# Kernel optimization log

Measured on AMD Instinct MI355X. Metric: run time of the kernel, lower is better.

The kernel has to match this reference:

```python
import jax, jax.numpy as jnp
import numpy as np

N = 20000   # nodes
E = 160000  # edges
D = 128     # out_dim == in_dim
H = 8       # heads
DK = D // H # 16


def setup_inputs() -> dict:
    key = jax.random.key(0)
    ks = jax.random.split(key, 16)
    f = lambda i, shape, s=1.0: jax.random.normal(ks[i], shape, dtype=jnp.float32) * s
    z = lambda shape: jnp.zeros(shape, dtype=jnp.float32)
    return {
        "x_txt": f(0, (N, D)), "x_img": f(1, (N, D)), "x_s": f(2, (N, D)),
        "Wk": f(3, (D, D), 0.05), "bk": z((D,)),
        "Wq": f(4, (D, D), 0.05), "bq": z((D,)),
        "Wv": f(5, (D, D), 0.05), "bv": z((D,)),
        "Wa": f(6, (D, D), 0.05), "ba": z((D,)),
        "rel_att": f(7, (H, DK, DK), 0.25),
        "rel_msg": f(8, (H, DK, DK), 0.25),
        "rel_pri": jnp.ones((H,), jnp.float32),
        "wm_txt": f(9, (H, DK, DK), 0.25),
        "wm_img": f(10, (H, DK, DK), 0.25),
        "wm_s": f(11, (H, DK, DK), 0.25),
        "skip": jnp.ones((1,), jnp.float32),
        "src": jax.random.randint(ks[12], (E,), 0, N),
        "dst": jax.random.randint(ks[13], (E,), 0, N),
    }


def reference(x_txt, x_img, x_s, Wk, bk, Wq, bq, Wv, bv, Wa, ba,
              rel_att, rel_msg, rel_pri, wm_txt, wm_img, wm_s, skip, src, dst):
    n_heads, dk = rel_att.shape[0], rel_att.shape[1]
    n_nodes = x_txt.shape[0]
    sqrt_dk = jnp.sqrt(jnp.asarray(dk, jnp.float32))

    def proj(x, W, b):
        return (x @ W + b).reshape(n_nodes, n_heads, dk)

    xs = (x_txt, x_img, x_s)
    k = [proj(x, Wk, bk)[src] for x in xs]  # [E,H,dk] gathered at src
    q = [proj(x, Wq, bq)[dst] for x in xs]  # [E,H,dk] gathered at dst
    v = [proj(x, Wv, bv)[src] for x in xs]

    # cross-modal lambda: per-edge modality alignment softmax (over the 3 modalities)
    wm = (wm_txt, wm_img, wm_s)
    lam_scores = jnp.stack(
        [jnp.einsum('ehd,hdf,ehf->eh', k[m], wm[m], q[m]) for m in range(3)], axis=0)
    lam = jax.nn.softmax(lam_scores, axis=0)  # [3,E,H]

    # edge attention logits (scaled *10 as in reduce_func) and relation-msg values
    att = [jnp.einsum('ehd,hdf,ehf->eh', k[m], rel_att, q[m]) * rel_pri / sqrt_dk * 10.0
           for m in range(3)]
    vmsg = [jnp.einsum('ehd,hdf->ehf', v[m], rel_msg) for m in range(3)]

    align = -(jnp.abs(att[0] - att[1]) + jnp.abs(att[0] - att[2])
              + jnp.abs(att[1] - att[2])) / 3.0

    def seg_softmax(x):  # softmax over edges sharing the same dst node
        m = jax.ops.segment_max(x, dst, num_segments=n_nodes)
        m = jnp.where(jnp.isfinite(m), m, 0.0)
        e = jnp.exp(x - m[dst])
        s = jax.ops.segment_sum(e, dst, num_segments=n_nodes)
        s = jnp.where(s == 0.0, 1.0, s)
        return e / s[dst]

    beta2 = seg_softmax(align)
    sm = [seg_softmax(a) for a in att]
    beta1 = sm[0] * lam[0] + sm[1] * lam[1] + sm[2] * lam[2]
    beta = seg_softmax(beta1 * beta2)  # [E,H]

    alpha = jax.nn.sigmoid(skip)  # [1]
    outs = []
    for m in range(3):
        h = jax.ops.segment_sum(beta[..., None] * vmsg[m], dst,
                                num_segments=n_nodes).reshape(n_nodes, -1)
        outs.append((h @ Wa + ba) * alpha + xs[m] * (1.0 - alpha))
    return tuple(outs)
```

## Files before the change

### kernel.cpp

```cpp
#include <hip/hip_runtime.h>

#define D 128
#define NH 8

typedef __bf16 bf16x8 __attribute__((ext_vector_type(8)));
typedef unsigned short ushortx8 __attribute__((ext_vector_type(8)));
typedef float floatx4 __attribute__((ext_vector_type(4)));

__device__ __forceinline__ float bf2f(unsigned short u) {
  union { unsigned int i; float f; } x; x.i = ((unsigned int)u) << 16; return x.f;
}
__device__ __forceinline__ unsigned short f2bf(float f) {
  union { float f; unsigned int i; } x; x.f = f;
  unsigned int i = x.i;
  return (unsigned short)((i + 0x7FFFu + ((i >> 16) & 1u)) >> 16);
}
__device__ __forceinline__ void acc2(unsigned int ku, unsigned int qu, float& s) {
  union { unsigned int i; float f; } a, b;
  a.i = ku << 16;          b.i = qu << 16;          s += a.f * b.f;
  a.i = ku & 0xffff0000u;  b.i = qu & 0xffff0000u;  s += a.f * b.f;
}

__device__ __forceinline__ void fold_item(
    int gid,
    const float* __restrict__ Wk, const float* __restrict__ bk,
    const float* __restrict__ Wq, const float* __restrict__ bq,
    const float* __restrict__ Wv, const float* __restrict__ bv,
    const float* __restrict__ rel_att, const float* __restrict__ rel_msg,
    const float* __restrict__ rel_pri,
    const float* __restrict__ wm0, const float* __restrict__ wm1,
    const float* __restrict__ wm2,
    unsigned short* __restrict__ Wt_all, float* __restrict__ bias_all)
{
  int p = gid >> 14;
  int idx = gid & 16383;
  int c = idx >> 7, k = idx & 127;
  int h = c >> 4, r = c & 15;
  float wsum = 0.f, bsum = 0.f;
  if (p == 0) {
    wsum = Wk[k * 128 + c];
    bsum = bk[c];
  } else if (p <= 4) {
    const float* M = (p == 1) ? rel_att : ((p == 2) ? wm0 : ((p == 3) ? wm1 : wm2));
#pragma unroll
    for (int f = 0; f < 16; f++) {
      float mv = M[h * 256 + r * 16 + f];
      wsum += Wq[k * 128 + h * 16 + f] * mv;
      bsum += bq[h * 16 + f] * mv;
    }
    if (p == 1) { float sc = rel_pri[h] * 2.5f; wsum *= sc; bsum *= sc; }
  } else {
#pragma unroll
    for (int d = 0; d < 16; d++) {
      float mv = rel_msg[h * 256 + d * 16 + r];
      wsum += Wv[k * 128 + h * 16 + d] * mv;
      bsum += bv[h * 16 + d] * mv;
    }
  }
  Wt_all[(size_t)p * 16384 + c * 128 + k] = f2bf(wsum);
  if (k == 0) bias_all[p * 128 + c] = bsum;
}

__device__ __forceinline__ void proj_tile(
    int t, const float* __restrict__ x0, const float* __restrict__ x1,
    const float* __restrict__ x2,
    const unsigned short* __restrict__ Wt_all, const float* __restrict__ bias_all,
    unsigned short* __restrict__ P, int N, unsigned short* Wt, int tid)
{
  int m = t % 3, rt = t / 3;
  const float* X = (m == 0) ? x0 : ((m == 1) ? x1 : x2);
  int wave = tid >> 6, lane = tid & 63;
  int quad = lane >> 4, l16 = lane & 15;
  int row0 = rt * 64 + wave * 16;
  int arow = row0 + l16; if (arow >= N) arow = N - 1;
  const float* ap = X + (size_t)arow * D;
  bf16x8 afr[4];
#pragma unroll
  for (int kk4 = 0; kk4 < 4; kk4++) {
    float4 f0 = *(const float4*)(ap + kk4 * 32 + quad * 8);
    float4 f1 = *(const float4*)(ap + kk4 * 32 + quad * 8 + 4);
    ushortx8 uu;
    uu[0]=f2bf(f0.x); uu[1]=f2bf(f0.y); uu[2]=f2bf(f0.z); uu[3]=f2bf(f0.w);
    uu[4]=f2bf(f1.x); uu[5]=f2bf(f1.y); uu[6]=f2bf(f1.z); uu[7]=f2bf(f1.w);
    afr[kk4] = __builtin_bit_cast(bf16x8, uu);
  }
  int r = row0 + l16;
  for (int pt = 0; pt < 4; pt++) {
    int wp = (pt == 0) ? 0 : ((pt == 1) ? 1 : ((pt == 2) ? (2 + m) : 5));
    const unsigned short* Wsrc = Wt_all + (size_t)wp * 16384;
    const float* B = bias_all + wp * 128;
    unsigned short* Pout = P + (size_t)(pt * 3 + m) * N * D;
    __syncthreads();
#pragma unroll
    for (int it = 0; it < 8; it++) {
      int idx = it * 256 + tid;
      int c = idx >> 4, kc = (idx & 15) << 3;
      *(uint4*)(&Wt[c * 136 + kc]) = *(const uint4*)(&Wsrc[c * 128 + kc]);
    }
    __syncthreads();
    floatx4 acc[8];
#pragma unroll
    for (int ct = 0; ct < 8; ct++) acc[ct] = (floatx4)0.f;
#pragma unroll
    for (int kk4 = 0; kk4 < 4; kk4++) {
#pragma unroll
      for (int ct2 = 0; ct2 < 8; ct2++) {
        uint4 bu = *(const uint4*)(&Wt[(ct2 * 16 + l16) * 136 + kk4 * 32 + quad * 8]);
        bf16x8 bf = __builtin_bit_cast(bf16x8, bu);
        acc[ct2] =
            __builtin_amdgcn_mfma_f32_16x16x32_bf16(bf, afr[kk4], acc[ct2], 0, 0, 0);
      }
    }
    if (r < N) {
      unsigned short* Prow = Pout + (size_t)r * D;
#pragma unroll
      for (int ct2 = 0; ct2 < 8; ct2++) {
        int colb = ct2 * 16 + quad * 4;
        float4 bi = *(const float4*)(&B[colb]);
        unsigned int lo = ((unsigned int)f2bf(acc[ct2][1] + bi.y) << 16) |
                          f2bf(acc[ct2][0] + bi.x);
        unsigned int hi = ((unsigned int)f2bf(acc[ct2][3] + bi.w) << 16) |
                          f2bf(acc[ct2][2] + bi.z);
        uint2 pk; pk.x = lo; pk.y = hi;
        *(uint2*)(&Prow[colb]) = pk;
      }
    }
  }
}

__device__ __forceinline__ void assign_chunk(
    int a, const int* __restrict__ counts, int* __restrict__ row_start,
    int* __restrict__ cursor, int* __restrict__ allocg, int N, int lane)
{
  int n = a * 64 + lane;
  int cnt = (n < N) ? counts[n] : 0;
  int x = cnt;
#pragma unroll
  for (int off = 1; off < 64; off <<= 1) {
    int y = __shfl_up(x, off, 64);
    if (lane >= off) x += y;
  }
  int wtot = __shfl(x, 63, 64);
  int wbase = 0;
  if (lane == 63) wbase = atomicAdd(allocg, wtot);
  wbase = __shfl(wbase, 63, 64);
  if (n < N) { int v = wbase + x - cnt; row_start[n] = v; cursor[n] = v; }
}

__device__ __forceinline__ void edge_vals(
    const unsigned short* __restrict__ P, size_t Nsz, int s, int h,
    const uint4 (&qa)[3][2], const uint4 (&qw)[3][2],
    float (&av)[3], float (&lv)[3])
{
#pragma unroll
  for (int m = 0; m < 3; m++) {
    const unsigned short* kp = P + ((size_t)m * Nsz + s) * 128 + h * 16;
    uint4 k0 = *(const uint4*)kp, k1 = *(const uint4*)(kp + 8);
    const unsigned int* ka = (const unsigned int*)&k0;
    const unsigned int* kb = (const unsigned int*)&k1;
    const unsigned int* a0 = (const unsigned int*)&qa[m][0];
    const unsigned int* a1 = (const unsigned int*)&qa[m][1];
    const unsigned int* w0 = (const unsigned int*)&qw[m][0];
    const unsigned int* w1 = (const unsigned int*)&qw[m][1];
    float da = 0.f, dw = 0.f;
#pragma unroll
    for (int j = 0; j < 4; j++) {
      acc2(ka[j], a0[j], da); acc2(kb[j], a1[j], da);
      acc2(ka[j], w0[j], dw); acc2(kb[j], w1[j], dw);
    }
    av[m] = da;
    lv[m] = dw;
  }
  float mx = fmaxf(lv[0], fmaxf(lv[1], lv[2]));
  float e0 = __expf(lv[0] - mx), e1 = __expf(lv[1] - mx), e2 = __expf(lv[2] - mx);
  float inv = 1.f / (e0 + e1 + e2);
  lv[0] = e0 * inv; lv[1] = e1 * inv; lv[2] = e2 * inv;
}

__device__ __forceinline__ void node_one(
    int n, const unsigned short* __restrict__ P,
    const int* __restrict__ row_start, const int* __restrict__ counts,
    const int* __restrict__ srcs, unsigned short* __restrict__ hagg,
    int N, int lane)
{
  int ro = row_start[n];
  int deg = counts[n];
  float acc00 = 0, acc01 = 0, acc10 = 0, acc11 = 0, acc20 = 0, acc21 = 0;
  if (deg > 0) {
    int h = lane & 7, slot = lane >> 3;
    size_t Nsz = (size_t)N;
    uint4 qa[3][2], qw[3][2];
#pragma unroll
    for (int m = 0; m < 3; m++) {
      const unsigned short* qap = P + ((size_t)(3 + m) * Nsz + n) * 128 + h * 16;
      const unsigned short* qwp = P + ((size_t)(6 + m) * Nsz + n) * 128 + h * 16;
      qa[m][0] = *(const uint4*)qap; qa[m][1] = *(const uint4*)(qap + 8);
      qw[m][0] = *(const uint4*)qwp; qw[m][1] = *(const uint4*)(qwp + 8);
    }
    int nch = (deg + 7) >> 3;
    float cX0[4] = {}, cX1[4] = {}, cX2[4] = {}, cEa[4] = {}, cT[4] = {};
    int cS[4] = {};
    float sA0 = 0, sA1 = 0, sA2 = 0, sAl = 0;
#pragma unroll
    for (int c = 0; c < 4; c++) {
      int idx = c * 8 + slot;
      if (c < nch && idx < deg) {
        int s = srcs[ro + idx]; cS[c] = s;
        float av[3], lv[3];
        edge_vals(P, Nsz, s, h, qa, qw, av, lv);
        float e0 = __expf(av[0]), e1 = __expf(av[1]), e2 = __expf(av[2]);
        float align = -(fabsf(av[0]-av[1]) + fabsf(av[0]-av[2]) + fabsf(av[1]-av[2])) * (1.f/3.f);
        float ea = __expf(align);
        cX0[c] = lv[0] * e0; cX1[c] = lv[1] * e1; cX2[c] = lv[2] * e2; cEa[c] = ea;
        sA0 += e0; sA1 += e1; sA2 += e2; sAl += ea;
      }
    }
    for (int c = 4; c < nch; c++) {
      int idx = c * 8 + slot;
      if (idx < deg) {
        int s = srcs[ro + idx];
        float av[3], lv[3];
        edge_vals(P, Nsz, s, h, qa, qw, av, lv);
        float align = -(fabsf(av[0]-av[1]) + fabsf(av[0]-av[2]) + fabsf(av[1]-av[2])) * (1.f/3.f);
        sA0 += __expf(av[0]); sA1 += __expf(av[1]); sA2 += __expf(av[2]);
        sAl += __expf(align);
      }
    }
#pragma unroll
    for (int off = 8; off < 64; off <<= 1) {
      sA0 += __shfl_xor(sA0, off, 64);
      sA1 += __shfl_xor(sA1, off, 64);
      sA2 += __shfl_xor(sA2, off, 64);
      sAl += __shfl_xor(sAl, off, 64);
    }
    float rA0 = 1.f / fmaxf(sA0, 1e-30f), rA1 = 1.f / fmaxf(sA1, 1e-30f);
    float rA2 = 1.f / fmaxf(sA2, 1e-30f), rAl = 1.f / fmaxf(sAl, 1e-30f);
    float sT = 0;
#pragma unroll
    for (int c = 0; c < 4; c++) {
      int idx = c * 8 + slot;
      if (c < nch && idx < deg) {
        float t = (cX0[c] * rA0 + cX1[c] * rA1 + cX2[c] * rA2) * (cEa[c] * rAl);
        cT[c] = t;
        sT += __expf(t);
      }
    }
    for (int c = 4; c < nch; c++) {
      int idx = c * 8 + slot;
      if (idx < deg) {
        int s = srcs[ro + idx];
        float av[3], lv[3];
        edge_vals(P, Nsz, s, h, qa, qw, av, lv);
        float align = -(fabsf(av[0]-av[1]) + fabsf(av[0]-av[2]) + fabsf(av[1]-av[2])) * (1.f/3.f);
        float t = (lv[0]*__expf(av[0])*rA0 + lv[1]*__expf(av[1])*rA1 + lv[2]*__expf(av[2])*rA2)
                  * (__expf(align) * rAl);
        sT += __expf(t);
      }
    }
#pragma unroll
    for (int off = 8; off < 64; off <<= 1) sT += __shfl_xor(sT, off, 64);
    float rT = 1.f / fmaxf(sT, 1e-30f);
    const unsigned int* Pu = (const unsigned int*)P;
    int hl = lane >> 3;
#pragma unroll
    for (int c = 0; c < 4; c++) {
      if (c < nch) {
        int idx = c * 8 + slot;
        float beta = (idx < deg) ? __expf(cT[c]) * rT : 0.f;
        int sv = cS[c];
        float bj[8]; int sj[8];
#pragma unroll
        for (int jj = 0; jj < 8; jj++) {
          bj[jj] = __shfl(beta, jj * 8 + hl, 64);
          sj[jj] = __shfl(sv, jj * 8, 64);
        }
#pragma unroll
        for (int jj = 0; jj < 8; jj++) {
          size_t base9 = ((size_t)9 * Nsz + sj[jj]) * 64 + lane;
          unsigned int u0 = Pu[base9];
          unsigned int u1 = Pu[base9 + Nsz * 64];
          unsigned int u2 = Pu[base9 + 2 * Nsz * 64];
          float b = bj[jj];
          acc00 += b * bf2f((unsigned short)u0); acc01 += b * bf2f((unsigned short)(u0 >> 16));
          acc10 += b * bf2f((unsigned short)u1); acc11 += b * bf2f((unsigned short)(u1 >> 16));
          acc20 += b * bf2f((unsigned short)u2); acc21 += b * bf2f((unsigned short)(u2 >> 16));
        }
      }
    }
    for (int c = 4; c < nch; c++) {
      int idx = c * 8 + slot;
      float beta = 0.f; int sv = 0;
      if (idx < deg) {
        sv = srcs[ro + idx];
        float av[3], lv[3];
        edge_vals(P, Nsz, sv, h, qa, qw, av, lv);
        float align = -(fabsf(av[0]-av[1]) + fabsf(av[0]-av[2]) + fabsf(av[1]-av[2])) * (1.f/3.f);
        float t = (lv[0]*__expf(av[0])*rA0 + lv[1]*__expf(av[1])*rA1 + lv[2]*__expf(av[2])*rA2)
                  * (__expf(align) * rAl);
        beta = __expf(t) * rT;
      }
      int jmax = min(8, deg - c * 8);
      for (int jj = 0; jj < jmax; jj++) {
        float b = __shfl(beta, jj * 8 + hl, 64);
        int s = __shfl(sv, jj * 8, 64);
        size_t base9 = ((size_t)9 * Nsz + s) * 64 + lane;
        unsigned int u0 = Pu[base9];
        unsigned int u1 = Pu[base9 + Nsz * 64];
        unsigned int u2 = Pu[base9 + 2 * Nsz * 64];
        acc00 += b * bf2f((unsigned short)u0); acc01 += b * bf2f((unsigned short)(u0 >> 16));
        acc10 += b * bf2f((unsigned short)u1); acc11 += b * bf2f((unsigned short)(u1 >> 16));
        acc20 += b * bf2f((unsigned short)u2); acc21 += b * bf2f((unsigned short)(u2 >> 16));
      }
    }
  }
  unsigned int* ho = (unsigned int*)hagg;
  ho[((size_t)0 * N + n) * 64 + lane] = ((unsigned int)f2bf(acc01) << 16) | f2bf(acc00);
  ho[((size_t)1 * N + n) * 64 + lane] = ((unsigned int)f2bf(acc11) << 16) | f2bf(acc10);
  ho[((size_t)2 * N + n) * 64 + lane] = ((unsigned int)f2bf(acc21) << 16) | f2bf(acc20);
}

__device__ __forceinline__ void out_tile(
    int t, const unsigned short* __restrict__ Hagg,
    const float* __restrict__ ba,
    const float* __restrict__ x0, const float* __restrict__ x1,
    const float* __restrict__ x2, float alpha,
    float* __restrict__ out, int N, const unsigned short* Wt, int tid)
{
  int m = t % 3, rt = t / 3;
  const float* X = (m == 0) ? x0 : ((m == 1) ? x1 : x2);
  float oma = 1.f - alpha;
  int wave = tid >> 6, lane = tid & 63;
  int quad = lane >> 4, l16 = lane & 15;
  int row0 = rt * 64 + wave * 16;
  int arow = row0 + l16; if (arow >= N) arow = N - 1;
  const unsigned short* hp = Hagg + ((size_t)m * N + arow) * D;
  floatx4 acc[8];
#pragma unroll
  for (int ct = 0; ct < 8; ct++) acc[ct] = (floatx4)0.f;
#pragma unroll
  for (int kk = 0; kk < 128; kk += 32) {
    uint4 au = *(const uint4*)(hp + kk + quad * 8);
    bf16x8 af = __builtin_bit_cast(bf16x8, au);
#pragma unroll
    for (int ct = 0; ct < 8; ct++) {
      uint4 bu = *(const uint4*)(&Wt[(ct * 16 + l16) * 136 + kk + quad * 8]);
      bf16x8 bf = __builtin_bit_cast(bf16x8, bu);
      acc[ct] = __builtin_amdgcn_mfma_f32_16x16x32_bf16(bf, af, acc[ct], 0, 0, 0);
    }
  }
  int r = row0 + l16;
  if (r < N) {
    float* om = out + (size_t)m * N * D + (size_t)r * D;
    const float* xr = X + (size_t)r * D;
#pragma unroll
    for (int ct = 0; ct < 8; ct++) {
      int colb = ct * 16 + quad * 4;
      float4 bi = *(const float4*)(&ba[colb]);
      float4 xv = *(const float4*)(&xr[colb]);
      float4 res;
      res.x = (acc[ct][0] + bi.x) * alpha + xv.x * oma;
      res.y = (acc[ct][1] + bi.y) * alpha + xv.y * oma;
      res.z = (acc[ct][2] + bi.z) * alpha + xv.z * oma;
      res.w = (acc[ct][3] + bi.w) * alpha + xv.w * oma;
      *(float4*)(&om[colb]) = res;
    }
  }
}

__global__ __launch_bounds__(256) void fb_misc(
    const float* Wk, const float* bk, const float* Wq, const float* bq,
    const float* Wv, const float* bv,
    const float* rel_att, const float* rel_msg, const float* rel_pri,
    const float* wm0, const float* wm1, const float* wm2,
    unsigned short* Wt_all, float* bias_all,
    const int* dst, int* counts, int E)
{
  int b = blockIdx.x;
  if (b < 384) {
    int g = b * 256 + threadIdx.x;
    if (g < 6 * 16384)
      fold_item(g, Wk, bk, Wq, bq, Wv, bv, rel_att, rel_msg, rel_pri,
                wm0, wm1, wm2, Wt_all, bias_all);
  } else {
    int e = (b - 384) * 256 + threadIdx.x;
    if (e < E) atomicAdd(&counts[dst[e]], 1);
  }
}

__global__ __launch_bounds__(256) void fb_projassign(
    const float* x0, const float* x1, const float* x2,
    const unsigned short* Wt_all, const float* bias_all,
    unsigned short* P, const int* counts, int* row_start, int* cursor,
    int* allocg, int N)
{
  __shared__ __attribute__((aligned(16))) unsigned short Wt[128 * 136];
  int ntiles = ((N + 63) / 64) * 3;
  int b = blockIdx.x;
  if (b < ntiles) {
    proj_tile(b, x0, x1, x2, Wt_all, bias_all, P, N, Wt, threadIdx.x);
  } else {
    int a = (b - ntiles) * 4 + (threadIdx.x >> 6);
    if (a < (N + 63) / 64)
      assign_chunk(a, counts, row_start, cursor, allocg, N, threadIdx.x & 63);
  }
}

__global__ void fb_scatter(const int* dst, const int* src, int* cursor,
                           int* src_sorted, int E) {
  int e = blockIdx.x * 256 + threadIdx.x;
  if (e < E) {
    int d = dst[e];
    int pos = atomicAdd(&cursor[d], 1);
    src_sorted[pos] = src[e];
  }
}

__global__ __launch_bounds__(256) void fb_node(
    const unsigned short* P, const int* row_start, const int* counts,
    const int* srcs, unsigned short* hagg, int N)
{
  int n = blockIdx.x * 4 + (threadIdx.x >> 6);
  if (n < N) node_one(n, P, row_start, counts, srcs, hagg, N, threadIdx.x & 63);
}

__global__ __launch_bounds__(256) void fb_out(
    const unsigned short* Hagg, const float* Wa, const float* ba,
    const float* x0, const float* x1, const float* x2, const float* skip,
    float* out, int N)
{
  __shared__ __attribute__((aligned(16))) unsigned short Wt[128 * 136];
  int tid = threadIdx.x;
#pragma unroll
  for (int it = 0; it < 16; it++) {
    int idx = it * 256 + tid;
    int k = idx >> 5, c4 = (idx & 31) << 2;
    float4 w = *(const float4*)(&Wa[k * 128 + c4]);
    Wt[(c4 + 0) * 136 + k] = f2bf(w.x);
    Wt[(c4 + 1) * 136 + k] = f2bf(w.y);
    Wt[(c4 + 2) * 136 + k] = f2bf(w.z);
    Wt[(c4 + 3) * 136 + k] = f2bf(w.w);
  }
  __syncthreads();
  float alpha = 1.f / (1.f + __expf(-skip[0]));
  out_tile(blockIdx.x, Hagg, ba, x0, x1, x2, alpha, (float*)out, N, Wt, tid);
}

extern "C" void kernel_launch(void* const* d_in, const int* in_sizes, int n_in,
                              void* d_out, int out_size, void* d_ws, size_t ws_size,
                              hipStream_t stream) {
  const float* x0 = (const float*)d_in[0];
  const float* x1 = (const float*)d_in[1];
  const float* x2 = (const float*)d_in[2];
  const float* Wk = (const float*)d_in[3];
  const float* bk = (const float*)d_in[4];
  const float* Wq = (const float*)d_in[5];
  const float* bq = (const float*)d_in[6];
  const float* Wv = (const float*)d_in[7];
  const float* bv = (const float*)d_in[8];
  const float* Wa = (const float*)d_in[9];
  const float* ba = (const float*)d_in[10];
  const float* rel_att = (const float*)d_in[11];
  const float* rel_msg = (const float*)d_in[12];
  const float* rel_pri = (const float*)d_in[13];
  const float* wm0 = (const float*)d_in[14];
  const float* wm1 = (const float*)d_in[15];
  const float* wm2 = (const float*)d_in[16];
  const float* skip = (const float*)d_in[17];
  const int* src = (const int*)d_in[18];
  const int* dstv = (const int*)d_in[19];
  int N = in_sizes[0] / D;
  int E = in_sizes[18];

  char* wsb = (char*)d_ws;
  size_t off = 0;
  auto alloc_b = [&](size_t bytes) { size_t o = off; off += (bytes + 63) & ~(size_t)63; return o; };
  unsigned short* P         = (unsigned short*)(wsb + alloc_b((size_t)12 * N * D * 2));
  unsigned short* Wt_all    = (unsigned short*)(wsb + alloc_b((size_t)6 * 16384 * 2));
  float*          bias_all  = (float*)(wsb + alloc_b((size_t)6 * 128 * 4));
  int*            ctrl      = (int*)(wsb + alloc_b(((size_t)144 + 2 * N) * 4));
  int*            row_start = (int*)(wsb + alloc_b((size_t)(N + 1) * 4));
  int*            src_sorted= (int*)(wsb + alloc_b((size_t)E * 4));
  unsigned short* hagg      = (unsigned short*)(wsb + alloc_b((size_t)3 * N * D * 2));
  int* allocg = ctrl + 128;
  int* counts = ctrl + 144;
  int* cursor = ctrl + 144 + N;

  hipMemsetAsync(ctrl, 0, ((size_t)144 + N) * sizeof(int), stream);

  int ntiles = ((N + 63) / 64) * 3;
  int nchunks = (N + 63) / 64;
  fb_misc<<<dim3(384 + (E + 255) / 256), 256, 0, stream>>>(
      Wk, bk, Wq, bq, Wv, bv, rel_att, rel_msg, rel_pri, wm0, wm1, wm2,
      Wt_all, bias_all, dstv, counts, E);
  fb_projassign<<<dim3(ntiles + (nchunks + 3) / 4), 256, 0, stream>>>(
      x0, x1, x2, Wt_all, bias_all, P, counts, row_start, cursor, allocg, N);
  fb_scatter<<<dim3((E + 255) / 256), 256, 0, stream>>>(
      dstv, src, cursor, src_sorted, E);
  fb_node<<<dim3((N + 3) / 4), 256, 0, stream>>>(
      P, row_start, counts, src_sorted, hagg, N);
  fb_out<<<dim3(ntiles), 256, 0, stream>>>(
      hagg, Wa, ba, x0, x1, x2, skip, (float*)d_out, N);
}
```

Measured before the change: 241.9 us.

## Fuse node aggregation with output projection, keeping aggregated features in LDS

```diff
diff --git a/kernel.cpp b/kernel.cpp
--- a/kernel.cpp
+++ b/kernel.cpp
@@ -26,6 +26,7 @@
     const float* __restrict__ Wk, const float* __restrict__ bk,
     const float* __restrict__ Wq, const float* __restrict__ bq,
     const float* __restrict__ Wv, const float* __restrict__ bv,
+    const float* __restrict__ Wa,
     const float* __restrict__ rel_att, const float* __restrict__ rel_msg,
     const float* __restrict__ rel_pri,
     const float* __restrict__ wm0, const float* __restrict__ wm1,
@@ -49,13 +50,16 @@
       bsum += bq[h * 16 + f] * mv;
     }
     if (p == 1) { float sc = rel_pri[h] * 2.5f; wsum *= sc; bsum *= sc; }
-  } else {
+  } else if (p == 5) {
 #pragma unroll
     for (int d = 0; d < 16; d++) {
       float mv = rel_msg[h * 256 + d * 16 + r];
       wsum += Wv[k * 128 + h * 16 + d] * mv;
       bsum += bv[h * 16 + d] * mv;
     }
+  } else {
+    wsum = Wa[k * 128 + c];
+    bsum = 0.f;
   }
   Wt_all[(size_t)p * 16384 + c * 128 + k] = f2bf(wsum);
   if (k == 0) bias_all[p * 128 + c] = bsum;
@@ -180,8 +184,8 @@
 __device__ __forceinline__ void node_one(
     int n, const unsigned short* __restrict__ P,
     const int* __restrict__ row_start, const int* __restrict__ counts,
-    const int* __restrict__ srcs, unsigned short* __restrict__ hagg,
-    int N, int lane)
+    const int* __restrict__ srcs, unsigned short* __restrict__ Hs,
+    int N, int lane, int wave)
 {
   int ro = row_start[n];
   int deg = counts[n];
@@ -313,76 +317,30 @@
       }
     }
   }
-  unsigned int* ho = (unsigned int*)hagg;
-  ho[((size_t)0 * N + n) * 64 + lane] = ((unsigned int)f2bf(acc01) << 16) | f2bf(acc00);
-  ho[((size_t)1 * N + n) * 64 + lane] = ((unsigned int)f2bf(acc11) << 16) | f2bf(acc10);
-  ho[((size_t)2 * N + n) * 64 + lane] = ((unsigned int)f2bf(acc21) << 16) | f2bf(acc20);
-}
-
-__device__ __forceinline__ void out_tile(
-    int t, const unsigned short* __restrict__ Hagg,
-    const float* __restrict__ ba,
-    const float* __restrict__ x0, const float* __restrict__ x1,
-    const float* __restrict__ x2, float alpha,
-    float* __restrict__ out, int N, const unsigned short* Wt, int tid)
-{
-  int m = t % 3, rt = t / 3;
-  const float* X = (m == 0) ? x0 : ((m == 1) ? x1 : x2);
-  float oma = 1.f - alpha;
-  int wave = tid >> 6, lane = tid & 63;
-  int quad = lane >> 4, l16 = lane & 15;
-  int row0 = rt * 64 + wave * 16;
-  int arow = row0 + l16; if (arow >= N) arow = N - 1;
-  const unsigned short* hp = Hagg + ((size_t)m * N + arow) * D;
-  floatx4 acc[8];
-#pragma unroll
-  for (int ct = 0; ct < 8; ct++) acc[ct] = (floatx4)0.f;
-#pragma unroll
-  for (int kk = 0; kk < 128; kk += 32) {
-    uint4 au = *(const uint4*)(hp + kk + quad * 8);
-    bf16x8 af = __builtin_bit_cast(bf16x8, au);
-#pragma unroll
-    for (int ct = 0; ct < 8; ct++) {
-      uint4 bu = *(const uint4*)(&Wt[(ct * 16 + l16) * 136 + kk + quad * 8]);
-      bf16x8 bf = __builtin_bit_cast(bf16x8, bu);
-      acc[ct] = __builtin_amdgcn_mfma_f32_16x16x32_bf16(bf, af, acc[ct], 0, 0, 0);
-    }
-  }
-  int r = row0 + l16;
-  if (r < N) {
-    float* om = out + (size_t)m * N * D + (size_t)r * D;
-    const float* xr = X + (size_t)r * D;
-#pragma unroll
-    for (int ct = 0; ct < 8; ct++) {
-      int colb = ct * 16 + quad * 4;
-      float4 bi = *(const float4*)(&ba[colb]);
-      float4 xv = *(const float4*)(&xr[colb]);
-      float4 res;
-      res.x = (acc[ct][0] + bi.x) * alpha + xv.x * oma;
-      res.y = (acc[ct][1] + bi.y) * alpha + xv.y * oma;
-      res.z = (acc[ct][2] + bi.z) * alpha + xv.z * oma;
-      res.w = (acc[ct][3] + bi.w) * alpha + xv.w * oma;
-      *(float4*)(&om[colb]) = res;
-    }
-  }
+  *(unsigned int*)(&Hs[(0 * 4 + wave) * 136 + 2 * lane]) =
+      ((unsigned int)f2bf(acc01) << 16) | f2bf(acc00);
+  *(unsigned int*)(&Hs[(1 * 4 + wave) * 136 + 2 * lane]) =
+      ((unsigned int)f2bf(acc11) << 16) | f2bf(acc10);
+  *(unsigned int*)(&Hs[(2 * 4 + wave) * 136 + 2 * lane]) =
+      ((unsigned int)f2bf(acc21) << 16) | f2bf(acc20);
 }
 
 __global__ __launch_bounds__(256) void fb_misc(
     const float* Wk, const float* bk, const float* Wq, const float* bq,
-    const float* Wv, const float* bv,
+    const float* Wv, const float* bv, const float* Wa,
     const float* rel_att, const float* rel_msg, const float* rel_pri,
     const float* wm0, const float* wm1, const float* wm2,
     unsigned short* Wt_all, float* bias_all,
     const int* dst, int* counts, int E)
 {
   int b = blockIdx.x;
-  if (b < 384) {
+  if (b < 448) {
     int g = b * 256 + threadIdx.x;
-    if (g < 6 * 16384)
-      fold_item(g, Wk, bk, Wq, bq, Wv, bv, rel_att, rel_msg, rel_pri,
+    if (g < 7 * 16384)
+      fold_item(g, Wk, bk, Wq, bq, Wv, bv, Wa, rel_att, rel_msg, rel_pri,
                 wm0, wm1, wm2, Wt_all, bias_all);
   } else {
-    int e = (b - 384) * 256 + threadIdx.x;
+    int e = (b - 448) * 256 + threadIdx.x;
     if (e < E) atomicAdd(&counts[dst[e]], 1);
   }
 }
@@ -415,34 +373,72 @@
   }
 }
 
-__global__ __launch_bounds__(256) void fb_node(
+__global__ __launch_bounds__(256) void fb_node_out(
     const unsigned short* P, const int* row_start, const int* counts,
-    const int* srcs, unsigned short* hagg, int N)
-{
-  int n = blockIdx.x * 4 + (threadIdx.x >> 6);
-  if (n < N) node_one(n, P, row_start, counts, srcs, hagg, N, threadIdx.x & 63);
-}
-
-__global__ __launch_bounds__(256) void fb_out(
-    const unsigned short* Hagg, const float* Wa, const float* ba,
+    const int* srcs, const unsigned short* Wt_all, const float* ba,
     const float* x0, const float* x1, const float* x2, const float* skip,
     float* out, int N)
 {
-  __shared__ __attribute__((aligned(16))) unsigned short Wt[128 * 136];
-  int tid = threadIdx.x;
-#pragma unroll
-  for (int it = 0; it < 16; it++) {
+  __shared__ __attribute__((aligned(16))) unsigned short WtS[128 * 136];
+  __shared__ __attribute__((aligned(16))) unsigned short Hs[16 * 136];
+  int tid = threadIdx.x, wave = tid >> 6, lane = tid & 63;
+  const unsigned short* WaT = Wt_all + (size_t)6 * 16384;
+#pragma unroll
+  for (int it = 0; it < 8; it++) {
     int idx = it * 256 + tid;
-    int k = idx >> 5, c4 = (idx & 31) << 2;
-    float4 w = *(const float4*)(&Wa[k * 128 + c4]);
-    Wt[(c4 + 0) * 136 + k] = f2bf(w.x);
-    Wt[(c4 + 1) * 136 + k] = f2bf(w.y);
-    Wt[(c4 + 2) * 136 + k] = f2bf(w.z);
-    Wt[(c4 + 3) * 136 + k] = f2bf(w.w);
+    int c = idx >> 4, kc = (idx & 15) << 3;
+    *(uint4*)(&WtS[c * 136 + kc]) = *(const uint4*)(&WaT[c * 128 + kc]);
+  }
+  *(unsigned int*)(&Hs[(12 + wave) * 136 + 2 * lane]) = 0u;
+
+  int n = blockIdx.x * 4 + wave;
+  if (n < N)
+    node_one(n, P, row_start, counts, srcs, Hs, N, lane, wave);
+  else {
+    *(unsigned int*)(&Hs[(0 * 4 + wave) * 136 + 2 * lane]) = 0u;
+    *(unsigned int*)(&Hs[(1 * 4 + wave) * 136 + 2 * lane]) = 0u;
+    *(unsigned int*)(&Hs[(2 * 4 + wave) * 136 + 2 * lane]) = 0u;
   }
   __syncthreads();
-  float alpha = 1.f / (1.f + __expf(-skip[0]));
-  out_tile(blockIdx.x, Hagg, ba, x0, x1, x2, alpha, (float*)out, N, Wt, tid);
+
+  int quad = lane >> 4, l16 = lane & 15;
+  floatx4 oacc[2];
+  oacc[0] = (floatx4)0.f; oacc[1] = (floatx4)0.f;
+#pragma unroll
+  for (int kk = 0; kk < 128; kk += 32) {
+    uint4 au = *(const uint4*)(&Hs[l16 * 136 + kk + quad * 8]);
+    bf16x8 af = __builtin_bit_cast(bf16x8, au);
+#pragma unroll
+    for (int j = 0; j < 2; j++) {
+      int ct = wave * 2 + j;
+      uint4 bu = *(const uint4*)(&WtS[(ct * 16 + l16) * 136 + kk + quad * 8]);
+      bf16x8 bf = __builtin_bit_cast(bf16x8, bu);
+      oacc[j] = __builtin_amdgcn_mfma_f32_16x16x32_bf16(bf, af, oacc[j], 0, 0, 0);
+    }
+  }
+  if (l16 < 12) {
+    int m = l16 >> 2, wsrc = l16 & 3;
+    int n_out = blockIdx.x * 4 + wsrc;
+    if (n_out < N) {
+      float alpha = 1.f / (1.f + __expf(-skip[0]));
+      float oma = 1.f - alpha;
+      const float* X = (m == 0) ? x0 : ((m == 1) ? x1 : x2);
+      const float* xr = X + (size_t)n_out * D;
+      float* om = out + (size_t)m * N * D + (size_t)n_out * D;
+#pragma unroll
+      for (int j = 0; j < 2; j++) {
+        int colb = (wave * 2 + j) * 16 + quad * 4;
+        float4 bi = *(const float4*)(&ba[colb]);
+        float4 xv = *(const float4*)(&xr[colb]);
+        float4 res;
+        res.x = (oacc[j][0] + bi.x) * alpha + xv.x * oma;
+        res.y = (oacc[j][1] + bi.y) * alpha + xv.y * oma;
+        res.z = (oacc[j][2] + bi.z) * alpha + xv.z * oma;
+        res.w = (oacc[j][3] + bi.w) * alpha + xv.w * oma;
+        *(float4*)(&om[colb]) = res;
+      }
+    }
+  }
 }
 
 extern "C" void kernel_launch(void* const* d_in, const int* in_sizes, int n_in,
@@ -475,12 +471,11 @@
   size_t off = 0;
   auto alloc_b = [&](size_t bytes) { size_t o = off; off += (bytes + 63) & ~(size_t)63; return o; };
   unsigned short* P         = (unsigned short*)(wsb + alloc_b((size_t)12 * N * D * 2));
-  unsigned short* Wt_all    = (unsigned short*)(wsb + alloc_b((size_t)6 * 16384 * 2));
-  float*          bias_all  = (float*)(wsb + alloc_b((size_t)6 * 128 * 4));
+  unsigned short* Wt_all    = (unsigned short*)(wsb + alloc_b((size_t)7 * 16384 * 2));
+  float*          bias_all  = (float*)(wsb + alloc_b((size_t)7 * 128 * 4));
   int*            ctrl      = (int*)(wsb + alloc_b(((size_t)144 + 2 * N) * 4));
   int*            row_start = (int*)(wsb + alloc_b((size_t)(N + 1) * 4));
   int*            src_sorted= (int*)(wsb + alloc_b((size_t)E * 4));
-  unsigned short* hagg      = (unsigned short*)(wsb + alloc_b((size_t)3 * N * D * 2));
   int* allocg = ctrl + 128;
   int* counts = ctrl + 144;
   int* cursor = ctrl + 144 + N;
@@ -489,15 +484,14 @@
 
   int ntiles = ((N + 63) / 64) * 3;
   int nchunks = (N + 63) / 64;
-  fb_misc<<<dim3(384 + (E + 255) / 256), 256, 0, stream>>>(
-      Wk, bk, Wq, bq, Wv, bv, rel_att, rel_msg, rel_pri, wm0, wm1, wm2,
+  fb_misc<<<dim3(448 + (E + 255) / 256), 256, 0, stream>>>(
+      Wk, bk, Wq, bq, Wv, bv, Wa, rel_att, rel_msg, rel_pri, wm0, wm1, wm2,
       Wt_all, bias_all, dstv, counts, E);
   fb_projassign<<<dim3(ntiles + (nchunks + 3) / 4), 256, 0, stream>>>(
       x0, x1, x2, Wt_all, bias_all, P, counts, row_start, cursor, allocg, N);
   fb_scatter<<<dim3((E + 255) / 256), 256, 0, stream>>>(
       dstv, src, cursor, src_sorted, E);
-  fb_node<<<dim3((N + 3) / 4), 256, 0, stream>>>(
-      P, row_start, counts, src_sorted, hagg, N);
-  fb_out<<<dim3(ntiles), 256, 0, stream>>>(
-      hagg, Wa, ba, x0, x1, x2, skip, (float*)d_out, N);
-}
+  fb_node_out<<<dim3((N + 3) / 4), 256, 0, stream>>>(
+      P, row_start, counts, src_sorted, Wt_all, ba, x0, x1, x2, skip,
+      (float*)d_out, N);
+}
```

Result: faster. 233.9 us (-3.3%).
